# Kernel optimization log

Measured on AMD Instinct MI355X. Metric: run time of the kernel, lower is better.

Reference implementation:

```python
import jax, jax.numpy as jnp
import numpy as np
from jax import lax

B, T, D_IN, H, L = 256, 160, 40, 768, 3
SCALE = 0.05

def setup_inputs() -> dict:
    key = jax.random.key(0)
    ks = jax.random.split(key, 1 + 3 * L)
    inp = {"x": jax.random.normal(ks[0], (B, T, D_IN), dtype=jnp.float32)}
    in_dims = [D_IN, H, H]
    for l in range(L):
        inp[f"Wi{l}"] = jax.random.normal(ks[1 + 3 * l], (in_dims[l], 4 * H), dtype=jnp.float32) * SCALE
        inp[f"Wh{l}"] = jax.random.normal(ks[2 + 3 * l], (H, 4 * H), dtype=jnp.float32) * SCALE
        inp[f"b{l}"] = jnp.zeros((4 * H,), dtype=jnp.float32)
    return inp

def _lstm_layer(x, Wi, Wh, b):
    # x: [B, T, D]; returns [B, T, H]
    batch = x.shape[0]
    h_dim = Wh.shape[0]
    # Precompute input projections for all timesteps (big GEMM, compute-friendly)
    xw = jnp.einsum('btd,dh->bth', x, Wi) + b  # [B, T, 4H]
    c0 = jnp.zeros((batch, h_dim), dtype=x.dtype)
    h0 = jnp.zeros((batch, h_dim), dtype=x.dtype)

    def step(carry, xw_t):
        c, h = carry
        z = xw_t + h @ Wh  # [B, 4H]
        i, f, g, o = jnp.split(z, 4, axis=-1)  # flax LSTMCell gate order
        i = jax.nn.sigmoid(i)
        f = jax.nn.sigmoid(f)
        g = jnp.tanh(g)
        o = jax.nn.sigmoid(o)
        c_new = f * c + i * g
        h_new = o * jnp.tanh(c_new)
        return (c_new, h_new), h_new

    _, ys = lax.scan(step, (c0, h0), jnp.swapaxes(xw, 0, 1))  # ys: [T, B, H]
    return jnp.swapaxes(ys, 0, 1)

def reference(x, Wi0, Wh0, b0, Wi1, Wh1, b1, Wi2, Wh2, b2):
    h = _lstm_layer(x, Wi0, Wh0, b0)
    h = _lstm_layer(h, Wi1, Wh1, b1)
    h = _lstm_layer(h, Wi2, Wh2, b2)
    # frame_aggregation_mean = True -> mean over time
    return jnp.mean(h, axis=1)
```

## Files before the change

### kernel.cpp

```cpp
#include <hip/hip_runtime.h>
#include <stdint.h>

#define B_   256
#define T_   160
#define DIN_ 40
#define H_   768
#define NG_  3072
#define KP0_ 1024
#define KP12_ 1536
#define XC_  48

typedef _Float16 f16;
typedef _Float16 half8 __attribute__((ext_vector_type(8)));
typedef float f32x4 __attribute__((ext_vector_type(4)));

#define AS1C(p) ((const __attribute__((address_space(1))) uint32_t*)(p))
#define AS3(p)  ((__attribute__((address_space(3))) uint32_t*)(p))

struct Params {
  const f16* wt0; const f16* wt1; const f16* wt2;
  const float* bq; const f16* x16;
  f16* hs0; f16* hs1; f16* hs2;
  const f16* zpad; unsigned* cnt; float* out;
};

__device__ __forceinline__ float sigmoid_f(float x) { return 1.f / (1.f + __expf(-x)); }
__device__ __forceinline__ float tanh_f(float x) {
  x = fminf(15.f, fmaxf(-15.f, x));
  float e = __expf(2.f * x);
  return (e - 1.f) / (e + 1.f);
}

__global__ void conv_w(const float* __restrict__ Wi, const float* __restrict__ Wh,
                       int in_dim, int hoff, int Kp, f16* __restrict__ dst) {
  __shared__ f16 tile[64][66];
  const int k0 = blockIdx.x * 64;
  const int by = blockIdx.y;
  const int g = by / 12, j0 = (by % 12) * 64;
  const int tid = threadIdx.x;
  #pragma unroll
  for (int it = 0; it < 16; ++it) {
    int idx = it * 256 + tid;
    int jj = idx & 63;
    int kk = idx >> 6;
    int k = k0 + kk;
    int oc = g * H_ + j0 + jj;
    float v = 0.f;
    if (k < in_dim) v = Wi[(size_t)k * NG_ + oc];
    else if (k >= hoff && k < hoff + H_) v = Wh[(size_t)(k - hoff) * NG_ + oc];
    tile[kk][jj] = (f16)v;
  }
  __syncthreads();
  #pragma unroll
  for (int it = 0; it < 16; ++it) {
    int idx = it * 256 + tid;
    int kk = idx & 63;
    int jj = idx >> 6;
    int np = 4 * (j0 + jj) + g;
    dst[(size_t)np * Kp + k0 + kk] = tile[kk][jj];
  }
}

__global__ void conv_b(const float* __restrict__ b0, const float* __restrict__ b1,
                       const float* __restrict__ b2, float* __restrict__ bq) {
  int id = blockIdx.x * 256 + threadIdx.x;
  if (id < 3 * NG_) {
    int l = id / NG_, np = id % NG_;
    int j = np >> 2, g = np & 3;
    const float* s = (l == 0) ? b0 : (l == 1 ? b1 : b2);
    bq[id] = s[g * H_ + j];
  }
}

__global__ void conv_x(const float* __restrict__ x, f16* __restrict__ x16) {
  int id = blockIdx.x * 256 + threadIdx.x;
  if (id >= T_ * B_ * XC_) return;
  int k = id % XC_;
  int b = (id / XC_) % B_;
  int t = id / (XC_ * B_);
  float v = (k < DIN_) ? x[(size_t)b * (T_ * DIN_) + t * DIN_ + k] : 0.f;
  x16[id] = (f16)v;
}

template<int L>
__device__ __forceinline__ void run_layer(
    const f16* __restrict__ WT, const f16* __restrict__ hin, f16* __restrict__ hown,
    const float* __restrict__ bql, const f16* __restrict__ zpad, float* __restrict__ out,
    unsigned* cbar, unsigned& iter, f16* Abuf, float* zred, float* bqs,
    int tid, int lane, int w, int kw, int cw, int btile, int ntile, int n0) {
  constexpr int KP  = (L == 0) ? KP0_ : KP12_;
  constexpr int KQ  = KP / 4;
  constexpr int NKT = KQ / 32;
  constexpr int CH  = (L == 0) ? 128 : 96;

  if (tid < 96) bqs[tid] = bql[tid];

  half8 breg[3 * NKT];
  #pragma unroll
  for (int ct = 0; ct < 3; ++ct) {
    #pragma unroll
    for (int kt = 0; kt < NKT; ++kt) {
      int col = n0 + cw * 48 + ct * 16 + (lane & 15);
      int k = kw * KQ + kt * 32 + (lane >> 4) * 8;
      breg[ct * NKT + kt] = *(const half8*)(WT + (size_t)col * KP + k);
    }
  }

  auto stage_hin = [&](int slot) {
    #pragma unroll
    for (int i = 0; i < 24; ++i) {
      int cb = (w - 6) * 1536 + i * 64;
      int idx = cb + lane;
      int row = idx / 96;
      int c = idx - row * 96;
      int cg = c ^ (row & 7);
      int b = btile * 32 + row;
      const f16* src = hin + ((size_t)slot * B_ + b) * H_ + cg * 8;
      __builtin_amdgcn_global_load_lds(AS1C(src), AS3(Abuf + (size_t)cb * 8), 16, 0, 0);
    }
  };
  if (L > 0 && tid >= 384) stage_hin(1);

  const int id = tid;
  const int grow = id / 12, gjp = id - grow * 12;
  const int gb = btile * 32 + grow;
  const int ghc0 = ntile * 24 + 2 * gjp;
  float c0 = 0.f, c1 = 0.f, oa0 = 0.f, oa1 = 0.f;

  for (int t = 0; t < T_; ++t) {
    if (L == 0) {
      #pragma unroll
      for (int i = 0; i < 8; ++i) {
        int cb = w * 512 + i * 64;
        int idx = cb + lane;
        int row = idx >> 7;
        int c = idx & 127;
        int cg = c ^ (row & 7);
        int b = btile * 32 + row;
        const f16* src;
        if (cg < 6)        src = hin + ((size_t)t * B_ + b) * XC_ + cg * 8;
        else if (cg < 102) src = hown + ((size_t)t * B_ + b) * H_ + (cg - 6) * 8;
        else               src = zpad;
        __builtin_amdgcn_global_load_lds(AS1C(src), AS3(Abuf + (size_t)cb * 8), 16, 0, 0);
      }
    } else if (w >= 4) {
      #pragma unroll
      for (int i = 0; i < 12; ++i) {
        int cb = (w - 4) * 768 + i * 64;
        int idx = cb + lane;
        int row = idx / 96;
        int c = idx - row * 96;
        int cg = c ^ (row & 7);
        int b = btile * 32 + row;
        const f16* src = hown + ((size_t)t * B_ + b) * H_ + cg * 8;
        __builtin_amdgcn_global_load_lds(AS1C(src), AS3(Abuf + (size_t)(32 * 768 + cb * 8)), 16, 0, 0);
      }
    }
    asm volatile("s_waitcnt vmcnt(0)" ::: "memory");
    __syncthreads();

    f32x4 acc[2][3] = {};
    const char* Ab = (const char*)(Abuf + (L == 0 ? 0 : (kw >> 1) * 32 * 768));
    const int cbase = (L == 0) ? kw * 32 : (kw & 1) * 48;
    #pragma unroll
    for (int kt = 0; kt < NKT; ++kt) {
      int c = cbase + kt * 4 + (lane >> 4);
      int row0 = (lane & 15);
      half8 a0 = *(const half8*)(Ab + (size_t)row0 * (CH * 16) + (size_t)(c ^ (row0 & 7)) * 16);
      int row1 = 16 + (lane & 15);
      half8 a1 = *(const half8*)(Ab + (size_t)row1 * (CH * 16) + (size_t)(c ^ (row1 & 7)) * 16);
      #pragma unroll
      for (int ct = 0; ct < 3; ++ct) {
        acc[0][ct] = __builtin_amdgcn_mfma_f32_16x16x32_f16(a0, breg[ct * NKT + kt], acc[0][ct], 0, 0, 0);
        acc[1][ct] = __builtin_amdgcn_mfma_f32_16x16x32_f16(a1, breg[ct * NKT + kt], acc[1][ct], 0, 0, 0);
      }
    }

    {
      float* zr = zred + kw * 3072;
      #pragma unroll
      for (int rt = 0; rt < 2; ++rt) {
        #pragma unroll
        for (int ct = 0; ct < 3; ++ct) {
          int row = rt * 16 + (lane >> 4) * 4;
          int col = cw * 48 + ct * 16 + (lane & 15);
          #pragma unroll
          for (int r4 = 0; r4 < 4; ++r4)
            zr[(size_t)(row + r4) * 96 + col] = acc[rt][ct][r4];
        }
      }
    }
    __syncthreads();

    if (tid >= 384) {
      if (L > 0 && t + 1 < T_) stage_hin(t + 2);
    } else {
      const float* z = zred + (size_t)id * 8;
      f32x4 za = *(const f32x4*)(z)        + *(const f32x4*)(z + 3072)
               + *(const f32x4*)(z + 6144) + *(const f32x4*)(z + 9216);
      f32x4 zb = *(const f32x4*)(z + 4)        + *(const f32x4*)(z + 3076)
               + *(const f32x4*)(z + 6148)     + *(const f32x4*)(z + 9220);
      za += *(const f32x4*)(bqs + gjp * 8);
      zb += *(const f32x4*)(bqs + gjp * 8 + 4);
      float i0 = sigmoid_f(za[0]), f0 = sigmoid_f(za[1]), g0 = tanh_f(za[2]), o0 = sigmoid_f(za[3]);
      float i1 = sigmoid_f(zb[0]), f1 = sigmoid_f(zb[1]), g1 = tanh_f(zb[2]), o1 = sigmoid_f(zb[3]);
      float cn0 = f0 * c0 + i0 * g0;
      float cn1 = f1 * c1 + i1 * g1;
      c0 = cn0; c1 = cn1;
      float h0 = o0 * tanh_f(cn0);
      float h1 = o1 * tanh_f(cn1);
      f16 hh0 = (f16)h0, hh1 = (f16)h1;
      unsigned u = ((unsigned)__builtin_bit_cast(uint16_t, hh1) << 16)
                 |  (unsigned)__builtin_bit_cast(uint16_t, hh0);
      unsigned* hp = (unsigned*)(hown + ((size_t)(t + 1) * B_ + gb) * H_ + ghc0);
      __hip_atomic_store(hp, u, __ATOMIC_RELAXED, __HIP_MEMORY_SCOPE_AGENT);
      if (L == 2) {
        oa0 += h0; oa1 += h1;
        if (t == T_ - 1) {
          out[(size_t)gb * H_ + ghc0]     = oa0 * (1.f / T_);
          out[(size_t)gb * H_ + ghc0 + 1] = oa1 * (1.f / T_);
        }
      }
    }

    if (tid < 384) { asm volatile("s_waitcnt vmcnt(0)" ::: "memory"); }
    __syncthreads();
    ++iter;
    if (w == 5) {
      if (lane == 0)
        __hip_atomic_store(cbar + (size_t)ntile * 32, iter,
                           __ATOMIC_RELAXED, __HIP_MEMORY_SCOPE_AGENT);
      unsigned* fp = cbar + (size_t)(lane & 31) * 32;
      for (;;) {
        unsigned v = __hip_atomic_load(fp, __ATOMIC_RELAXED, __HIP_MEMORY_SCOPE_AGENT);
        if (__ballot(v >= iter) == ~0ull) break;
        __builtin_amdgcn_s_sleep(1);
      }
    }
    __syncthreads();
  }
}

__global__ __launch_bounds__(512, 2) void lstm_main(Params p) {
  __shared__ __align__(16) f16 Abuf[2 * 32 * 768];
  __shared__ __align__(16) float zred[4 * 32 * 96];
  __shared__ __align__(16) float bqs[96];

  const int tid = threadIdx.x;
  const int lane = tid & 63;
  const int w = tid >> 6;
  const int kw = w >> 1, cw = w & 1;
  const int bid = blockIdx.x;
  const int btile = bid >> 5;
  const int ntile = bid & 31;
  unsigned* cbar = p.cnt + (size_t)btile * 1024;
  const int n0 = ntile * 96;
  unsigned iter = 0;

  run_layer<0>(p.wt0, p.x16, p.hs0, p.bq + 0 * NG_ + n0, p.zpad, p.out, cbar, iter,
               Abuf, zred, bqs, tid, lane, w, kw, cw, btile, ntile, n0);
  run_layer<1>(p.wt1, p.hs0, p.hs1, p.bq + 1 * NG_ + n0, p.zpad, p.out, cbar, iter,
               Abuf, zred, bqs, tid, lane, w, kw, cw, btile, ntile, n0);
  run_layer<2>(p.wt2, p.hs1, p.hs2, p.bq + 2 * NG_ + n0, p.zpad, p.out, cbar, iter,
               Abuf, zred, bqs, tid, lane, w, kw, cw, btile, ntile, n0);
}

extern "C" void kernel_launch(void* const* d_in, const int* in_sizes, int n_in,
                              void* d_out, int out_size, void* d_ws, size_t ws_size,
                              hipStream_t stream) {
  const float* x   = (const float*)d_in[0];
  const float* Wi0 = (const float*)d_in[1];
  const float* Wh0 = (const float*)d_in[2];
  const float* b0  = (const float*)d_in[3];
  const float* Wi1 = (const float*)d_in[4];
  const float* Wh1 = (const float*)d_in[5];
  const float* b1  = (const float*)d_in[6];
  const float* Wi2 = (const float*)d_in[7];
  const float* Wh2 = (const float*)d_in[8];
  const float* b2  = (const float*)d_in[9];

  char* wsb = (char*)d_ws;
  size_t off = 0;
  auto nxt = [&](size_t sz) { char* p = wsb + off; off += (sz + 255) & ~(size_t)255; return p; };
  f16*      wt0  = (f16*)nxt((size_t)NG_ * KP0_ * 2);
  f16*      wt1  = (f16*)nxt((size_t)NG_ * KP12_ * 2);
  f16*      wt2  = (f16*)nxt((size_t)NG_ * KP12_ * 2);
  float*    bq   = (float*)nxt((size_t)3 * NG_ * 4);
  f16*      x16  = (f16*)nxt((size_t)T_ * B_ * XC_ * 2);
  f16*      hs0  = (f16*)nxt((size_t)(T_ + 1) * B_ * H_ * 2);
  f16*      hs1  = (f16*)nxt((size_t)(T_ + 1) * B_ * H_ * 2);
  f16*      hs2  = (f16*)nxt((size_t)(T_ + 1) * B_ * H_ * 2);
  f16*      zpad = (f16*)nxt(256);
  unsigned* cnt  = (unsigned*)nxt(8 * 1024 * 4);
  if (off > ws_size) return;

  const size_t slot_bytes = (size_t)B_ * H_ * 2;
  hipMemsetAsync(hs0, 0, slot_bytes, stream);
  hipMemsetAsync(hs1, 0, slot_bytes, stream);
  hipMemsetAsync(hs2, 0, slot_bytes, stream);
  hipMemsetAsync((void*)zpad, 0, 256, stream);
  hipMemsetAsync(cnt, 0, 8 * 1024 * 4, stream);

  hipLaunchKernelGGL(conv_w, dim3(KP0_ / 64, 48), dim3(256), 0, stream, Wi0, Wh0, DIN_, XC_, KP0_, wt0);
  hipLaunchKernelGGL(conv_w, dim3(KP12_ / 64, 48), dim3(256), 0, stream, Wi1, Wh1, H_, H_, KP12_, wt1);
  hipLaunchKernelGGL(conv_w, dim3(KP12_ / 64, 48), dim3(256), 0, stream, Wi2, Wh2, H_, H_, KP12_, wt2);
  hipLaunchKernelGGL(conv_b, dim3((3 * NG_ + 255) / 256), dim3(256), 0, stream, b0, b1, b2, bq);
  hipLaunchKernelGGL(conv_x, dim3((T_ * B_ * XC_ + 255) / 256), dim3(256), 0, stream, x, x16);

  Params prm{wt0, wt1, wt2, bq, x16, hs0, hs1, hs2, zpad, cnt, (float*)d_out};
  hipLaunchKernelGGL(lstm_main, dim3(256), dim3(512), 0, stream, prm);
}
```

Before: 6.005 ms.

## Map batch tiles to XCDs and keep per-step barrier traffic in local L2

```diff
diff --git a/kernel.cpp b/kernel.cpp
--- a/kernel.cpp
+++ b/kernel.cpp
@@ -21,7 +21,7 @@
   const f16* wt0; const f16* wt1; const f16* wt2;
   const float* bq; const f16* x16;
   f16* hs0; f16* hs1; f16* hs2;
-  const f16* zpad; unsigned* cnt; float* out;
+  const f16* zpad; unsigned* cnt; unsigned* claim; unsigned* ibar; float* out;
 };
 
 __device__ __forceinline__ float sigmoid_f(float x) { return 1.f / (1.f + __expf(-x)); }
@@ -82,11 +82,18 @@
   x16[id] = (f16)v;
 }
 
+__device__ __forceinline__ unsigned ld_l2(const unsigned* p) {
+  unsigned v;
+  asm volatile("global_load_dword %0, %1, off sc0\n\ts_waitcnt vmcnt(0)"
+               : "=v"(v) : "v"(p) : "memory");
+  return v;
+}
+
 template<int L>
 __device__ __forceinline__ void run_layer(
     const f16* __restrict__ WT, const f16* __restrict__ hin, f16* __restrict__ hown,
     const float* __restrict__ bql, const f16* __restrict__ zpad, float* __restrict__ out,
-    unsigned* cbar, unsigned& iter, f16* Abuf, float* zred, float* bqs,
+    unsigned* flg, unsigned& iter, f16* Abuf, float* zred, float* bqs,
     int tid, int lane, int w, int kw, int cw, int btile, int ntile, int n0) {
   constexpr int KP  = (L == 0) ? KP0_ : KP12_;
   constexpr int KQ  = KP / 4;
@@ -213,7 +220,7 @@
       unsigned u = ((unsigned)__builtin_bit_cast(uint16_t, hh1) << 16)
                  |  (unsigned)__builtin_bit_cast(uint16_t, hh0);
       unsigned* hp = (unsigned*)(hown + ((size_t)(t + 1) * B_ + gb) * H_ + ghc0);
-      __hip_atomic_store(hp, u, __ATOMIC_RELAXED, __HIP_MEMORY_SCOPE_AGENT);
+      __hip_atomic_store(hp, u, __ATOMIC_RELAXED, __HIP_MEMORY_SCOPE_WORKGROUP);
       if (L == 2) {
         oa0 += h0; oa1 += h1;
         if (t == T_ - 1) {
@@ -228,12 +235,16 @@
     ++iter;
     if (w == 5) {
       if (lane == 0)
-        __hip_atomic_store(cbar + (size_t)ntile * 32, iter,
-                           __ATOMIC_RELAXED, __HIP_MEMORY_SCOPE_AGENT);
-      unsigned* fp = cbar + (size_t)(lane & 31) * 32;
+        __hip_atomic_store(flg + (size_t)ntile * 32, iter,
+                           __ATOMIC_RELAXED, __HIP_MEMORY_SCOPE_WORKGROUP);
+      unsigned* fp = flg + (size_t)(lane & 31) * 32;
+      int spins = 0;
       for (;;) {
-        unsigned v = __hip_atomic_load(fp, __ATOMIC_RELAXED, __HIP_MEMORY_SCOPE_AGENT);
+        unsigned v = (spins < 256)
+            ? ld_l2(fp)
+            : __hip_atomic_load(fp, __ATOMIC_RELAXED, __HIP_MEMORY_SCOPE_AGENT);
         if (__ballot(v >= iter) == ~0ull) break;
+        ++spins;
         __builtin_amdgcn_s_sleep(1);
       }
     }
@@ -245,23 +256,44 @@
   __shared__ __align__(16) f16 Abuf[2 * 32 * 768];
   __shared__ __align__(16) float zred[4 * 32 * 96];
   __shared__ __align__(16) float bqs[96];
+  __shared__ unsigned claim_s[2];
 
   const int tid = threadIdx.x;
   const int lane = tid & 63;
   const int w = tid >> 6;
   const int kw = w >> 1, cw = w & 1;
-  const int bid = blockIdx.x;
-  const int btile = bid >> 5;
-  const int ntile = bid & 31;
-  unsigned* cbar = p.cnt + (size_t)btile * 1024;
+
+  if (tid == 0) {
+    unsigned xcc;
+    asm volatile("s_getreg_b32 %0, hwreg(HW_REG_XCC_ID)" : "=s"(xcc));
+    xcc &= 7u;
+    unsigned slot = __hip_atomic_fetch_add(p.claim + xcc, 1u,
+                                           __ATOMIC_RELAXED, __HIP_MEMORY_SCOPE_AGENT);
+    claim_s[0] = xcc;
+    claim_s[1] = slot & 31u;
+  }
+  __syncthreads();
+  const int btile = (int)claim_s[0];
+  const int ntile = (int)claim_s[1];
+  unsigned* flg = p.cnt + (size_t)btile * 1024;
   const int n0 = ntile * 96;
   unsigned iter = 0;
 
-  run_layer<0>(p.wt0, p.x16, p.hs0, p.bq + 0 * NG_ + n0, p.zpad, p.out, cbar, iter,
+  if (tid == 0) {
+    __hip_atomic_store(flg + (size_t)ntile * 32, 0u,
+                       __ATOMIC_RELAXED, __HIP_MEMORY_SCOPE_WORKGROUP);
+    asm volatile("s_waitcnt vmcnt(0)" ::: "memory");
+    __hip_atomic_fetch_add(p.ibar + btile, 1u, __ATOMIC_RELEASE, __HIP_MEMORY_SCOPE_AGENT);
+    while (__hip_atomic_load(p.ibar + btile, __ATOMIC_RELAXED, __HIP_MEMORY_SCOPE_AGENT) < 32u)
+      __builtin_amdgcn_s_sleep(2);
+  }
+  __syncthreads();
+
+  run_layer<0>(p.wt0, p.x16, p.hs0, p.bq + 0 * NG_ + n0, p.zpad, p.out, flg, iter,
                Abuf, zred, bqs, tid, lane, w, kw, cw, btile, ntile, n0);
-  run_layer<1>(p.wt1, p.hs0, p.hs1, p.bq + 1 * NG_ + n0, p.zpad, p.out, cbar, iter,
+  run_layer<1>(p.wt1, p.hs0, p.hs1, p.bq + 1 * NG_ + n0, p.zpad, p.out, flg, iter,
                Abuf, zred, bqs, tid, lane, w, kw, cw, btile, ntile, n0);
-  run_layer<2>(p.wt2, p.hs1, p.hs2, p.bq + 2 * NG_ + n0, p.zpad, p.out, cbar, iter,
+  run_layer<2>(p.wt2, p.hs1, p.hs2, p.bq + 2 * NG_ + n0, p.zpad, p.out, flg, iter,
                Abuf, zred, bqs, tid, lane, w, kw, cw, btile, ntile, n0);
 }
 
@@ -292,6 +324,8 @@
   f16*      hs2  = (f16*)nxt((size_t)(T_ + 1) * B_ * H_ * 2);
   f16*      zpad = (f16*)nxt(256);
   unsigned* cnt  = (unsigned*)nxt(8 * 1024 * 4);
+  unsigned* claim= (unsigned*)nxt(256);
+  unsigned* ibar = (unsigned*)nxt(256);
   if (off > ws_size) return;
 
   const size_t slot_bytes = (size_t)B_ * H_ * 2;
@@ -300,6 +334,8 @@
   hipMemsetAsync(hs2, 0, slot_bytes, stream);
   hipMemsetAsync((void*)zpad, 0, 256, stream);
   hipMemsetAsync(cnt, 0, 8 * 1024 * 4, stream);
+  hipMemsetAsync(claim, 0, 256, stream);
+  hipMemsetAsync(ibar, 0, 256, stream);
 
   hipLaunchKernelGGL(conv_w, dim3(KP0_ / 64, 48), dim3(256), 0, stream, Wi0, Wh0, DIN_, XC_, KP0_, wt0);
   hipLaunchKernelGGL(conv_w, dim3(KP12_ / 64, 48), dim3(256), 0, stream, Wi1, Wh1, H_, H_, KP12_, wt1);
@@ -307,6 +343,6 @@
   hipLaunchKernelGGL(conv_b, dim3((3 * NG_ + 255) / 256), dim3(256), 0, stream, b0, b1, b2, bq);
   hipLaunchKernelGGL(conv_x, dim3((T_ * B_ * XC_ + 255) / 256), dim3(256), 0, stream, x, x16);
 
-  Params prm{wt0, wt1, wt2, bq, x16, hs0, hs1, hs2, zpad, cnt, (float*)d_out};
+  Params prm{wt0, wt1, wt2, bq, x16, hs0, hs1, hs2, zpad, cnt, claim, ibar, (float*)d_out};
   hipLaunchKernelGGL(lstm_main, dim3(256), dim3(512), 0, stream, prm);
 }
```

Result: slower. 19.32 ms (+221.8%).
